# Optimization experiments

Measured on AMD Instinct MI355X. Metric: run time of the kernel, lower is better.

The kernel has to match this reference:

```python
import jax, jax.numpy as jnp
import numpy as np

HIDDEN = 4096
N_HEADS = 32
N_KV = 32
HEAD_DIM = 128
T = 2048
EPS = 1e-5
ROPE_THETA = 1000000.0


def rms_norm(x, w, eps=EPS):
    var = jnp.mean(x * x, axis=-1, keepdims=True)
    return x * jax.lax.rsqrt(var + eps) * w


def apply_rope(x, positions):
    # x: [T, H, D] ; neox-style (rotate halves), full rotary_dim = HEAD_DIM
    half = HEAD_DIM // 2
    inv_freq = 1.0 / (ROPE_THETA ** (jnp.arange(0, half, dtype=jnp.float32) / half))
    ang = positions.astype(jnp.float32)[:, None] * inv_freq  # [T, half]
    cos = jnp.cos(ang)[:, None, :]  # [T, 1, half]
    sin = jnp.sin(ang)[:, None, :]
    x1, x2 = x[..., :half], x[..., half:]
    return jnp.concatenate([x1 * cos - x2 * sin, x2 * cos + x1 * sin], axis=-1)


def setup_inputs() -> dict:
    key = jax.random.key(0)
    ks = jax.random.split(key, 5)
    s = 0.02
    qkv_out = (N_HEADS + 2 * N_KV) * HEAD_DIM
    return {
        "hidden_states": jax.random.normal(ks[0], (T, HIDDEN), jnp.float32),
        "positions": jnp.arange(T, dtype=jnp.int32),
        "w_qkv": jax.random.normal(ks[1], (qkv_out, HIDDEN), jnp.float32) * s,
        "b_qkv": jax.random.normal(ks[2], (qkv_out,), jnp.float32) * s,
        "q_norm_w": jnp.ones((N_HEADS * HEAD_DIM,), jnp.float32),
        "k_norm_w": jnp.ones((N_KV * HEAD_DIM,), jnp.float32),
        "w_o": jax.random.normal(ks[3], (HIDDEN, N_HEADS * HEAD_DIM), jnp.float32) * s,
    }


def reference(hidden_states, positions, w_qkv, b_qkv, q_norm_w, k_norm_w, w_o):
    q_size = N_HEADS * HEAD_DIM
    kv_size = N_KV * HEAD_DIM
    qkv = hidden_states @ w_qkv.T + b_qkv  # [T, q+2kv]
    q, k, v = jnp.split(qkv, [q_size, q_size + kv_size], axis=-1)
    # QK RMSNorm over the full flattened q / k widths (as in Molmo)
    q = rms_norm(q, q_norm_w)
    k = rms_norm(k, k_norm_w)
    q = apply_rope(q.reshape(T, N_HEADS, HEAD_DIM), positions)
    k = apply_rope(k.reshape(T, N_KV, HEAD_DIM), positions)
    v = v.reshape(T, N_KV, HEAD_DIM)
    scale = HEAD_DIM ** -0.5
    scores = jnp.einsum("qhd,khd->hqk", q, k) * scale  # [H, T, T]
    causal = positions[:, None] >= positions[None, :]
    scores = jnp.where(causal[None], scores, jnp.float32(-1e30))
    probs = jax.nn.softmax(scores, axis=-1)
    attn = jnp.einsum("hqk,khd->qhd", probs, v).reshape(T, N_HEADS * HEAD_DIM)
    return attn @ w_o.T
```

## Files before the change

### kernel.cpp

```cpp
#include <hip/hip_runtime.h>
#include <hip/hip_bf16.h>

#define T_SEQ 2048
#define NH 32
#define HD 128
#define QKV_N 12288
#define V_OFF 8192

typedef __bf16 bf16;
typedef __attribute__((ext_vector_type(4))) __bf16 bf16x4;
typedef __attribute__((ext_vector_type(8))) __bf16 bf16x8;
typedef __attribute__((ext_vector_type(4))) float f32x4;

#define GLDS16(g, l)                                                        \
  __builtin_amdgcn_global_load_lds(                                         \
      (const __attribute__((address_space(1))) void*)(g),                   \
      (__attribute__((address_space(3))) void*)(l), 16, 0, 0)

__device__ inline bf16x8 load8(const bf16* p) { return *(const bf16x8*)p; }
__device__ inline bf16x8 load8(const float* p) {
    f32x4 a = *(const f32x4*)p;
    f32x4 b = *(const f32x4*)(p + 4);
    bf16x8 r;
    r[0] = (bf16)a[0]; r[1] = (bf16)a[1]; r[2] = (bf16)a[2]; r[3] = (bf16)a[3];
    r[4] = (bf16)b[0]; r[5] = (bf16)b[1]; r[6] = (bf16)b[2]; r[7] = (bf16)b[3];
    return r;
}

__global__ __launch_bounds__(256)
void f32_to_bf16(const float* __restrict__ in, bf16* __restrict__ out, int n8)
{
    for (int i = blockIdx.x * 256 + threadIdx.x; i < n8; i += gridDim.x * 256)
        *(bf16x8*)(out + (size_t)i * 8) = load8(in + (size_t)i * 8);
}

template <typename TO>
__global__ __launch_bounds__(512, 1)
void gemm_bt_256(const bf16* __restrict__ A, int lda,
                 const bf16* __restrict__ B,
                 const float* __restrict__ bias,
                 TO* __restrict__ C, int ldc,
                 int mTiles, int colPerXcd, int K)
{
    __shared__ bf16 lds[65536];
    bf16* ldsA = lds;
    bf16* ldsB = lds + 32768;

    const int tid  = threadIdx.x;
    const int wave = tid >> 6, lane = tid & 63;
    const int quad = lane >> 4, l16 = lane & 15;
    const int wm = wave >> 2, wn = wave & 3;

    const int b   = blockIdx.x;
    const int xcd = b & 7, i = b >> 3;
    const int rowBase = (i % mTiles) * 256;
    const int colBase = (xcd * colPerXcd + i / mTiles) * 256;
    const int nK = K >> 5;

    const bf16* gA[2];
    const bf16* gB[2];
#pragma unroll
    for (int j = 0; j < 2; ++j) {
        int c = j * 512 + tid;
        int d = c * 16;
        int s = d ^ ((d >> 3) & 0x70);
        int row = s >> 6;
        int ke  = (s & 63) >> 1;
        gA[j] = A + (size_t)(rowBase + row) * lda + ke;
        gB[j] = B + (size_t)(colBase + row) * K + ke;
    }

    int offA[8], offB[4];
#pragma unroll
    for (int mi = 0; mi < 8; ++mi) {
        int a = (wm * 128 + mi * 16 + l16) * 64 + quad * 16;
        offA[mi] = (a ^ ((a >> 3) & 0x70)) >> 1;
    }
#pragma unroll
    for (int ni = 0; ni < 4; ++ni) {
        int a = (wn * 64 + ni * 16 + l16) * 64 + quad * 16;
        offB[ni] = (a ^ ((a >> 3) & 0x70)) >> 1;
    }

    auto stageA = [&](int kt) {
        int sl = kt & 3;
#pragma unroll
        for (int j = 0; j < 2; ++j)
            GLDS16(gA[j] + kt * 32, ldsA + sl * 8192 + (j * 512 + wave * 64) * 8);
    };
    auto stageB = [&](int kt) {
        int sl = kt & 3;
#pragma unroll
        for (int j = 0; j < 2; ++j)
            GLDS16(gB[j] + kt * 32, ldsB + sl * 8192 + (j * 512 + wave * 64) * 8);
    };

    f32x4 acc[8][4] = {};

    stageA(0); stageB(0);
    stageA(1); stageB(1);
    stageA(2); stageB(2);
    asm volatile("s_waitcnt vmcnt(8)" ::: "memory");
    __builtin_amdgcn_s_barrier();

    for (int kt = 0; kt < nK; ++kt) {
        const int sl = kt & 3;
        const bf16* sA = ldsA + sl * 8192;
        const bf16* sB = ldsB + sl * 8192;
        bf16x8 af[4], bfr[4], af2[4];

#pragma unroll
        for (int mi = 0; mi < 4; ++mi) af[mi]  = *(const bf16x8*)(sA + offA[mi]);
#pragma unroll
        for (int ni = 0; ni < 4; ++ni) bfr[ni] = *(const bf16x8*)(sB + offB[ni]);
        if (kt + 3 < nK) stageA(kt + 3);
        __builtin_amdgcn_s_barrier();
        asm volatile("s_waitcnt lgkmcnt(0)" ::: "memory");
        __builtin_amdgcn_sched_barrier(0);
        __builtin_amdgcn_s_setprio(1);
#pragma unroll
        for (int mi = 0; mi < 4; ++mi)
#pragma unroll
            for (int ni = 0; ni < 4; ++ni)
                acc[mi][ni] = __builtin_amdgcn_mfma_f32_16x16x32_bf16(
                    af[mi], bfr[ni], acc[mi][ni], 0, 0, 0);
        __builtin_amdgcn_s_setprio(0);
        __builtin_amdgcn_s_barrier();

#pragma unroll
        for (int mi = 0; mi < 4; ++mi) af2[mi] = *(const bf16x8*)(sA + offA[4 + mi]);
        if (kt + 3 < nK) stageB(kt + 3);
        __builtin_amdgcn_s_barrier();
        asm volatile("s_waitcnt lgkmcnt(0)" ::: "memory");
        __builtin_amdgcn_sched_barrier(0);
        __builtin_amdgcn_s_setprio(1);
#pragma unroll
        for (int mi = 0; mi < 4; ++mi)
#pragma unroll
            for (int ni = 0; ni < 4; ++ni)
                acc[4 + mi][ni] = __builtin_amdgcn_mfma_f32_16x16x32_bf16(
                    af2[mi], bfr[ni], acc[4 + mi][ni], 0, 0, 0);
        __builtin_amdgcn_s_setprio(0);
        if (kt + 1 < nK) {
            if (kt + 3 < nK)      asm volatile("s_waitcnt vmcnt(8)" ::: "memory");
            else if (kt + 2 < nK) asm volatile("s_waitcnt vmcnt(4)" ::: "memory");
            else                  asm volatile("s_waitcnt vmcnt(0)" ::: "memory");
        }
        __builtin_amdgcn_s_barrier();
    }

#pragma unroll
    for (int ni = 0; ni < 4; ++ni) {
        int col = colBase + wn * 64 + ni * 16 + l16;
        float bv = bias ? bias[col] : 0.0f;
#pragma unroll
        for (int mi = 0; mi < 8; ++mi) {
            int row0 = rowBase + wm * 128 + mi * 16 + quad * 4;
#pragma unroll
            for (int r = 0; r < 4; ++r)
                C[(size_t)(row0 + r) * ldc + col] = (TO)(acc[mi][ni][r] + bv);
        }
    }
}

#define BM 128
#define BN 128
#define BK 32

template <typename TO>
__global__ __launch_bounds__(256, 2)
void gemm_bt_glds(const bf16* __restrict__ A, int lda,
                  const bf16* __restrict__ B,
                  const float* __restrict__ bias,
                  TO* __restrict__ C, int ldc,
                  int mTiles, int colPerXcd, int K)
{
    __shared__ bf16 sA[BM * BK];
    __shared__ bf16 sB[BN * BK];
    const int tid  = threadIdx.x;
    const int wave = tid >> 6, lane = tid & 63;
    const int quad = lane >> 4, l16 = lane & 15;
    const int wm = wave >> 1, wn = wave & 1;

    int b = blockIdx.x;
    int xcd = b & 7, i = b >> 3;
    const int rowBase = (i % mTiles) * BM;
    const int colBase = (xcd * colPerXcd + i / mTiles) * BN;

    f32x4 acc[4][4] = {};

    for (int k0 = 0; k0 < K; k0 += BK) {
        __syncthreads();
        for (int r = 0; r < 2; ++r) {
            int cb = wave * 128 + r * 64;
            int c  = cb + lane;
            int row = c >> 2, kg = c & 3;
            GLDS16(A + (size_t)(rowBase + row) * lda + k0 + kg * 8, sA + cb * 8);
            GLDS16(B + (size_t)(colBase + row) * K + k0 + kg * 8, sB + cb * 8);
        }
        __syncthreads();

        bf16x8 af[4], bfr[4];
        for (int mi = 0; mi < 4; ++mi)
            af[mi] = *(const bf16x8*)(sA + (wm * 64 + mi * 16 + l16) * BK + quad * 8);
        for (int ni = 0; ni < 4; ++ni)
            bfr[ni] = *(const bf16x8*)(sB + (wn * 64 + ni * 16 + l16) * BK + quad * 8);
        for (int mi = 0; mi < 4; ++mi)
            for (int ni = 0; ni < 4; ++ni)
                acc[mi][ni] = __builtin_amdgcn_mfma_f32_16x16x32_bf16(
                    af[mi], bfr[ni], acc[mi][ni], 0, 0, 0);
    }

    for (int ni = 0; ni < 4; ++ni) {
        int col = colBase + wn * 64 + ni * 16 + l16;
        float bv = bias ? bias[col] : 0.0f;
        for (int mi = 0; mi < 4; ++mi) {
            int row0 = rowBase + wm * 64 + mi * 16 + quad * 4;
            for (int r = 0; r < 4; ++r)
                C[(size_t)(row0 + r) * ldc + col] = (TO)(acc[mi][ni][r] + bv);
        }
    }
}

template <typename TA, typename TB, typename TO>
__global__ __launch_bounds__(256, 2)
void gemm_bt_bias(const TA* __restrict__ A, int lda,
                  const TB* __restrict__ B,
                  const float* __restrict__ bias,
                  TO* __restrict__ C, int ldc,
                  int M, int N, int K)
{
    __shared__ bf16 sA[BM * BK];
    __shared__ bf16 sB[BN * BK];
    const int tid  = threadIdx.x;
    const int wave = tid >> 6, lane = tid & 63;
    const int quad = lane >> 4, l16 = lane & 15;
    const int wm = wave >> 1, wn = wave & 1;
    const int rowBase = blockIdx.x * BM;
    const int colBase = blockIdx.y * BN;

    int c0 = wave * 128 + lane;
    int rowA0 = c0 >> 2, kgA0 = c0 & 3;
    int rowA1 = (c0 + 64) >> 2, kgA1 = (c0 + 64) & 3;

    f32x4 acc[4][4] = {};

    for (int k0 = 0; k0 < K; k0 += BK) {
        bf16x8 ra0 = load8(A + (size_t)(rowBase + rowA0) * lda + k0 + kgA0 * 8);
        bf16x8 ra1 = load8(A + (size_t)(rowBase + rowA1) * lda + k0 + kgA1 * 8);
        bf16x8 rb0 = load8(B + (size_t)(colBase + rowA0) * K + k0 + kgA0 * 8);
        bf16x8 rb1 = load8(B + (size_t)(colBase + rowA1) * K + k0 + kgA1 * 8);
        __syncthreads();
        *(bf16x8*)(sA + rowA0 * BK + kgA0 * 8) = ra0;
        *(bf16x8*)(sA + rowA1 * BK + kgA1 * 8) = ra1;
        *(bf16x8*)(sB + rowA0 * BK + kgA0 * 8) = rb0;
        *(bf16x8*)(sB + rowA1 * BK + kgA1 * 8) = rb1;
        __syncthreads();

        bf16x8 af[4], bfr[4];
        for (int mi = 0; mi < 4; ++mi)
            af[mi] = *(const bf16x8*)(sA + (wm * 64 + mi * 16 + l16) * BK + quad * 8);
        for (int ni = 0; ni < 4; ++ni)
            bfr[ni] = *(const bf16x8*)(sB + (wn * 64 + ni * 16 + l16) * BK + quad * 8);
        for (int mi = 0; mi < 4; ++mi)
            for (int ni = 0; ni < 4; ++ni)
                acc[mi][ni] = __builtin_amdgcn_mfma_f32_16x16x32_bf16(
                    af[mi], bfr[ni], acc[mi][ni], 0, 0, 0);
    }

    for (int ni = 0; ni < 4; ++ni) {
        int col = colBase + wn * 64 + ni * 16 + l16;
        float bv = bias ? bias[col] : 0.0f;
        for (int mi = 0; mi < 4; ++mi) {
            int row0 = rowBase + wm * 64 + mi * 16 + quad * 4;
            for (int r = 0; r < 4; ++r)
                C[(size_t)(row0 + r) * ldc + col] = (TO)(acc[mi][ni][r] + bv);
        }
    }
}

__global__ __launch_bounds__(256)
void rmsnorm_rope(bf16* __restrict__ qkv, const float* __restrict__ qw,
                  const float* __restrict__ kw, const int* __restrict__ pos)
{
    const int t   = blockIdx.x;
    const int sel = blockIdx.y;
    bf16* x = qkv + (size_t)t * QKV_N + sel * 4096;
    const float* w = sel ? kw : qw;
    const int tid = threadIdx.x;

    float ss = 0.f;
    {
        int i0 = tid * 16;
        bf16x8 a = *(const bf16x8*)(x + i0);
        bf16x8 b = *(const bf16x8*)(x + i0 + 8);
        for (int j = 0; j < 8; ++j) { float fa = (float)a[j]; ss += fa * fa; }
        for (int j = 0; j < 8; ++j) { float fb = (float)b[j]; ss += fb * fb; }
    }
    for (int off = 1; off < 64; off <<= 1) ss += __shfl_xor(ss, off, 64);
    __shared__ float red[4];
    if ((tid & 63) == 0) red[tid >> 6] = ss;
    __syncthreads();
    float tot = red[0] + red[1] + red[2] + red[3];
    float rstd = rsqrtf(tot * (1.0f / 4096.0f) + 1e-5f);

    float fp = (float)pos[t];
    for (int i = tid; i < 2048; i += 256) {
        int h = i >> 6;
        int d = i & 63;
        int base = h * 128 + d;
        float x1 = (float)x[base]      * rstd * w[base];
        float x2 = (float)x[base + 64] * rstd * w[base + 64];
        float ang = fp * exp2f(-(float)d * 0.31143075889569023f);
        float s, c;
        sincosf(ang, &s, &c);
        x[base]      = (bf16)(x1 * c - x2 * s);
        x[base + 64] = (bf16)(x2 * c + x1 * s);
    }
}

__global__ __launch_bounds__(256)
void v_transpose(const bf16* __restrict__ qkv, bf16* __restrict__ vt)
{
    __shared__ bf16 tile[64][65];
    int t0 = blockIdx.x * 64, d0 = blockIdx.y * 64, h = blockIdx.z;
    int x = threadIdx.x & 63, y4 = threadIdx.x >> 6;
    for (int yy = y4; yy < 64; yy += 4)
        tile[yy][x] = qkv[(size_t)(t0 + yy) * QKV_N + V_OFF + h * HD + d0 + x];
    __syncthreads();
    for (int yy = y4; yy < 64; yy += 4)
        vt[(size_t)(h * HD + d0 + yy) * T_SEQ + t0 + x] = tile[x][yy];
}

#define SKP 136
#define SVP 72
#define PBP 72

__global__ __launch_bounds__(256, 2)
void flash_attn(bf16* qkv, const bf16* vt)
{
    __shared__ bf16 sK[64 * SKP];
    __shared__ bf16 sV[128 * SVP];
    __shared__ bf16 pbuf[4 * 16 * PBP];

    const int tid  = threadIdx.x;
    const int wave = tid >> 6, lane = tid & 63;
    const int quad = lane >> 4, l16 = lane & 15;
    const int h    = blockIdx.y;

    const float sc = 0.08838834764831845f * 1.4426950408889634f;
    bf16* pb = pbuf + wave * 16 * PBP;

    for (int half = 0; half < 2; ++half) {
        const int blk  = half ? (31 - (int)blockIdx.x) : (int)blockIdx.x;
        const int q0w  = blk * 64 + wave * 16;
        const int kend = blk * 64;
        const int qln  = q0w + l16;

        bf16x8 qf[4];
        {
            const bf16* qrow = qkv + (size_t)qln * QKV_N + h * HD;
            for (int c = 0; c < 4; ++c)
                qf[c] = *(const bf16x8*)(qrow + c * 32 + quad * 8);
        }

        f32x4 oacc[8] = {};
        float m2 = -1e30f, lsum = 0.f;

        for (int kb = 0; kb <= kend; kb += 64) {
            __syncthreads();
            for (int j = 0; j < 4; ++j) {
                int c = tid + j * 256;
                int r = c >> 4, off = (c & 15) * 8;
                bf16x8 v = *(const bf16x8*)(qkv + (size_t)(kb + r) * QKV_N + 4096 + h * HD + off);
                *(bf16x8*)(sK + r * SKP + off) = v;
            }
            for (int j = 0; j < 4; ++j) {
                int c = tid + j * 256;
                int d = c >> 3, off = (c & 7) * 8;
                bf16x8 v = *(const bf16x8*)(vt + (size_t)(h * HD + d) * T_SEQ + kb + off);
                *(bf16x8*)(sV + d * SVP + off) = v;
            }
            __syncthreads();

            const int stmax = (kb == kend) ? (wave + 1) : 4;

            f32x4 s[4] = {};
            for (int st = 0; st < 4; ++st) {
                if (st >= stmax) break;
                const bf16* kbase = sK + (st * 16 + l16) * SKP + quad * 8;
                for (int c = 0; c < 4; ++c) {
                    bf16x8 kf = *(const bf16x8*)(kbase + c * 32);
                    s[st] = __builtin_amdgcn_mfma_f32_16x16x32_bf16(kf, qf[c], s[st], 0, 0, 0);
                }
            }
            for (int st = 0; st < 4; ++st) {
                int k0r = kb + st * 16 + quad * 4;
                for (int r = 0; r < 4; ++r) {
                    float v = s[st][r] * sc;
                    s[st][r] = (k0r + r <= qln) ? v : -1e30f;
                }
            }
            float mx = -1e30f;
            for (int st = 0; st < 4; ++st)
                for (int r = 0; r < 4; ++r) mx = fmaxf(mx, s[st][r]);
            mx = fmaxf(mx, __shfl_xor(mx, 16, 64));
            mx = fmaxf(mx, __shfl_xor(mx, 32, 64));
            float mnew  = fmaxf(m2, mx);
            float alpha = exp2f(m2 - mnew);
            float ps = 0.f;
            for (int st = 0; st < 4; ++st)
                for (int r = 0; r < 4; ++r) {
                    float p = exp2f(s[st][r] - mnew);
                    s[st][r] = p;
                    ps += p;
                }
            ps += __shfl_xor(ps, 16, 64);
            ps += __shfl_xor(ps, 32, 64);
            lsum = lsum * alpha + ps;
            m2 = mnew;

            float ar[4];
            for (int r = 0; r < 4; ++r) ar[r] = __shfl(alpha, quad * 4 + r, 64);
            for (int c = 0; c < 8; ++c)
                for (int r = 0; r < 4; ++r) oacc[c][r] *= ar[r];

            for (int st = 0; st < 4; ++st) {
                bf16x4 pw;
                for (int r = 0; r < 4; ++r) pw[r] = (bf16)s[st][r];
                *(bf16x4*)(pb + l16 * PBP + st * 16 + quad * 4) = pw;
            }
            __builtin_amdgcn_s_waitcnt(0xC07F);
            for (int ph = 0; ph < 2; ++ph) {
                bf16x8 pf = *(const bf16x8*)(pb + l16 * PBP + ph * 32 + quad * 8);
                for (int c = 0; c < 8; ++c) {
                    bf16x8 vf = *(const bf16x8*)(sV + (c * 16 + l16) * SVP + ph * 32 + quad * 8);
                    oacc[c] = __builtin_amdgcn_mfma_f32_16x16x32_bf16(pf, vf, oacc[c], 0, 0, 0);
                }
            }
        }

        float lr[4];
        for (int r = 0; r < 4; ++r) lr[r] = __shfl(lsum, quad * 4 + r, 64);
        for (int r = 0; r < 4; ++r) {
            float inv = 1.0f / lr[r];
            int t = q0w + quad * 4 + r;
            for (int c = 0; c < 8; ++c)
                qkv[(size_t)t * QKV_N + V_OFF + h * HD + c * 16 + l16] =
                    (bf16)(oacc[c][r] * inv);
        }
    }
}

extern "C" void kernel_launch(void* const* d_in, const int* in_sizes, int n_in,
                              void* d_out, int out_size, void* d_ws, size_t ws_size,
                              hipStream_t stream)
{
    const float* hidden   = (const float*)d_in[0];
    const int*   pos      = (const int*)d_in[1];
    const float* w_qkv    = (const float*)d_in[2];
    const float* b_qkv    = (const float*)d_in[3];
    const float* q_norm_w = (const float*)d_in[4];
    const float* k_norm_w = (const float*)d_in[5];
    const float* w_o      = (const float*)d_in[6];
    float* out = (float*)d_out;

    bf16* qkv = (bf16*)d_ws;
    bf16* vt  = qkv + (size_t)T_SEQ * QKV_N;
    bf16* wqb = vt  + (size_t)4096 * T_SEQ;
    bf16* wob = wqb + (size_t)QKV_N * 4096;
    bf16* hib = wob + (size_t)4096 * 4096;
    const size_t need = ((size_t)T_SEQ * QKV_N + (size_t)4096 * T_SEQ +
                         (size_t)QKV_N * 4096 + (size_t)4096 * 4096 +
                         (size_t)T_SEQ * 4096) * 2;

    if (ws_size >= need) {
        f32_to_bf16<<<2048, 256, 0, stream>>>(hidden, hib, T_SEQ * 4096 / 8);
        f32_to_bf16<<<8192, 256, 0, stream>>>(w_qkv, wqb, QKV_N * 4096 / 8);
        f32_to_bf16<<<4096, 256, 0, stream>>>(w_o, wob, 4096 * 4096 / 8);

        gemm_bt_256<bf16><<<8 * 8 * 6, 512, 0, stream>>>(
            hib, 4096, wqb, b_qkv, qkv, QKV_N, 8, 6, 4096);
        rmsnorm_rope<<<dim3(T_SEQ, 2), 256, 0, stream>>>(qkv, q_norm_w, k_norm_w, pos);
        v_transpose<<<dim3(T_SEQ / 64, 2, NH), 256, 0, stream>>>(qkv, vt);
        flash_attn<<<dim3(T_SEQ / 128, NH), 256, 0, stream>>>(qkv, vt);
        gemm_bt_glds<float><<<8 * 16 * 4, 256, 0, stream>>>(
            qkv + V_OFF, QKV_N, wob, nullptr, out, 4096, 16, 4, 4096);
    } else {
        gemm_bt_bias<float, float, bf16><<<dim3(T_SEQ / BM, QKV_N / BN), 256, 0, stream>>>(
            hidden, 4096, w_qkv, b_qkv, qkv, QKV_N, T_SEQ, QKV_N, 4096);
        rmsnorm_rope<<<dim3(T_SEQ, 2), 256, 0, stream>>>(qkv, q_norm_w, k_norm_w, pos);
        v_transpose<<<dim3(T_SEQ / 64, 2, NH), 256, 0, stream>>>(qkv, vt);
        flash_attn<<<dim3(T_SEQ / 128, NH), 256, 0, stream>>>(qkv, vt);
        gemm_bt_bias<bf16, float, float><<<dim3(T_SEQ / BM, 4096 / BN), 256, 0, stream>>>(
            qkv + V_OFF, QKV_N, w_o, nullptr, out, 4096, T_SEQ, 4096, 4096);
    }
}
```

Before: 836.7 us.

## Software-pipeline LDS fragment loads across k-steps in GEMM main loop

Restructures the GEMM main loop into a two-step unrolled, double-buffered register pipeline. Next k-tile A/B fragments are read from LDS while the second half of the current MFMAs runs, and both global-to-LDS stages are issued together at the start of each step. This cuts barriers per iteration from four to one and hides LDS latency behind MFMA work. It uses more registers, and the loop assumes nK is even; the lgkmcnt(8) wait must still line up with the LDS read order.

```diff
diff --git a/kernel.cpp b/kernel.cpp
--- a/kernel.cpp
+++ b/kernel.cpp
@@ -96,58 +96,74 @@
     };
 
     f32x4 acc[8][4] = {};
+    bf16x8 a47[4];
+    bf16x8 caX[4], cbX[4], caY[4], cbY[4];
 
     stageA(0); stageB(0);
     stageA(1); stageB(1);
     stageA(2); stageB(2);
     asm volatile("s_waitcnt vmcnt(8)" ::: "memory");
     __builtin_amdgcn_s_barrier();
-
-    for (int kt = 0; kt < nK; ++kt) {
-        const int sl = kt & 3;
-        const bf16* sA = ldsA + sl * 8192;
-        const bf16* sB = ldsB + sl * 8192;
-        bf16x8 af[4], bfr[4], af2[4];
-
-#pragma unroll
-        for (int mi = 0; mi < 4; ++mi) af[mi]  = *(const bf16x8*)(sA + offA[mi]);
-#pragma unroll
-        for (int ni = 0; ni < 4; ++ni) bfr[ni] = *(const bf16x8*)(sB + offB[ni]);
-        if (kt + 3 < nK) stageA(kt + 3);
-        __builtin_amdgcn_s_barrier();
-        asm volatile("s_waitcnt lgkmcnt(0)" ::: "memory");
-        __builtin_amdgcn_sched_barrier(0);
-        __builtin_amdgcn_s_setprio(1);
-#pragma unroll
-        for (int mi = 0; mi < 4; ++mi)
-#pragma unroll
-            for (int ni = 0; ni < 4; ++ni)
-                acc[mi][ni] = __builtin_amdgcn_mfma_f32_16x16x32_bf16(
-                    af[mi], bfr[ni], acc[mi][ni], 0, 0, 0);
-        __builtin_amdgcn_s_setprio(0);
-        __builtin_amdgcn_s_barrier();
-
-#pragma unroll
-        for (int mi = 0; mi < 4; ++mi) af2[mi] = *(const bf16x8*)(sA + offA[4 + mi]);
-        if (kt + 3 < nK) stageB(kt + 3);
-        __builtin_amdgcn_s_barrier();
-        asm volatile("s_waitcnt lgkmcnt(0)" ::: "memory");
-        __builtin_amdgcn_sched_barrier(0);
-        __builtin_amdgcn_s_setprio(1);
-#pragma unroll
-        for (int mi = 0; mi < 4; ++mi)
-#pragma unroll
-            for (int ni = 0; ni < 4; ++ni)
-                acc[4 + mi][ni] = __builtin_amdgcn_mfma_f32_16x16x32_bf16(
-                    af2[mi], bfr[ni], acc[4 + mi][ni], 0, 0, 0);
-        __builtin_amdgcn_s_setprio(0);
-        if (kt + 1 < nK) {
-            if (kt + 3 < nK)      asm volatile("s_waitcnt vmcnt(8)" ::: "memory");
-            else if (kt + 2 < nK) asm volatile("s_waitcnt vmcnt(4)" ::: "memory");
-            else                  asm volatile("s_waitcnt vmcnt(0)" ::: "memory");
-        }
-        __builtin_amdgcn_s_barrier();
-    }
+#pragma unroll
+    for (int mi = 0; mi < 4; ++mi) caX[mi] = *(const bf16x8*)(ldsA + offA[mi]);
+#pragma unroll
+    for (int ni = 0; ni < 4; ++ni) cbX[ni] = *(const bf16x8*)(ldsB + offB[ni]);
+
+#define GBODY(kt, CA, CB, NA, NB)                                             \
+  {                                                                           \
+    const bf16* sAc = ldsA + ((kt) & 3) * 8192;                               \
+    const bf16* sAn = ldsA + (((kt) + 1) & 3) * 8192;                         \
+    const bf16* sBn = ldsB + (((kt) + 1) & 3) * 8192;                         \
+    if ((kt) + 3 < nK) { stageA((kt) + 3); stageB((kt) + 3); }                \
+    asm volatile("s_waitcnt lgkmcnt(0)" ::: "memory");                        \
+    __builtin_amdgcn_sched_barrier(0);                                        \
+    _Pragma("unroll")                                                         \
+    for (int mi = 0; mi < 4; ++mi)                                            \
+        a47[mi] = *(const bf16x8*)(sAc + offA[4 + mi]);                       \
+    __builtin_amdgcn_sched_barrier(0);                                        \
+    __builtin_amdgcn_s_setprio(1);                                            \
+    _Pragma("unroll")                                                         \
+    for (int mi = 0; mi < 4; ++mi)                                            \
+        _Pragma("unroll")                                                     \
+        for (int ni = 0; ni < 4; ++ni)                                        \
+            acc[mi][ni] = __builtin_amdgcn_mfma_f32_16x16x32_bf16(            \
+                CA[mi], CB[ni], acc[mi][ni], 0, 0, 0);                        \
+    __builtin_amdgcn_s_setprio(0);                                            \
+    __builtin_amdgcn_sched_barrier(0);                                        \
+    if ((kt) + 1 < nK) {                                                      \
+        if ((kt) + 3 < nK)      asm volatile("s_waitcnt vmcnt(8)":::"memory");\
+        else if ((kt) + 2 < nK) asm volatile("s_waitcnt vmcnt(4)":::"memory");\
+        else                    asm volatile("s_waitcnt vmcnt(0)":::"memory");\
+    }                                                                         \
+    __builtin_amdgcn_s_barrier();                                             \
+    __builtin_amdgcn_sched_barrier(0);                                        \
+    if ((kt) + 1 < nK) {                                                      \
+        _Pragma("unroll")                                                     \
+        for (int mi = 0; mi < 4; ++mi)                                        \
+            NA[mi] = *(const bf16x8*)(sAn + offA[mi]);                        \
+        _Pragma("unroll")                                                     \
+        for (int ni = 0; ni < 4; ++ni)                                        \
+            NB[ni] = *(const bf16x8*)(sBn + offB[ni]);                        \
+        asm volatile("s_waitcnt lgkmcnt(8)" ::: "memory");                    \
+    } else {                                                                  \
+        asm volatile("s_waitcnt lgkmcnt(0)" ::: "memory");                    \
+    }                                                                         \
+    __builtin_amdgcn_sched_barrier(0);                                        \
+    __builtin_amdgcn_s_setprio(1);                                            \
+    _Pragma("unroll")                                                         \
+    for (int mi = 0; mi < 4; ++mi)                                            \
+        _Pragma("unroll")                                                     \
+        for (int ni = 0; ni < 4; ++ni)                                        \
+            acc[4 + mi][ni] = __builtin_amdgcn_mfma_f32_16x16x32_bf16(        \
+                a47[mi], CB[ni], acc[4 + mi][ni], 0, 0, 0);                   \
+    __builtin_amdgcn_s_setprio(0);                                            \
+  }
+
+    for (int kt = 0; kt < nK; kt += 2) {
+        GBODY(kt,     caX, cbX, caY, cbY);
+        GBODY(kt + 1, caY, cbY, caX, cbX);
+    }
+#undef GBODY
 
 #pragma unroll
     for (int ni = 0; ni < 4; ++ni) {
```

New measurement: 845.4 us. Within noise of the previous version (+1.0%).
